# Performance work log

Measured on AMD Instinct MI355X. Metric: run time of the kernel, lower is better.

## Reference

```python
import jax, jax.numpy as jnp
import numpy as np

N_DRUG = 846
E = 64          # embedding_num
S = 1024        # neighbor_sample_size
T_LEN = 50000   # tail entity vocab
R_LEN = 100     # relation vocab
BN_EPS = 1e-5


def setup_inputs() -> dict:
    key = jax.random.key(0)
    ks = jax.random.split(key, 12)
    inp = {
        'drug_name': jnp.arange(N_DRUG, dtype=jnp.int64) if jax.config.jax_enable_x64 else jnp.arange(N_DRUG, dtype=jnp.int32),
        'adj_tail': jax.random.randint(ks[0], (N_DRUG, S), 0, T_LEN),
        'adj_relation': jax.random.randint(ks[1], (N_DRUG, S), 0, R_LEN),
        # learned parameters
        'drug_table': jax.random.normal(ks[2], (N_DRUG, E), jnp.float32),
        'rela_table': jax.random.normal(ks[3], (R_LEN, E), jnp.float32),
        'ent_table': jax.random.normal(ks[4], (T_LEN, E), jnp.float32),
        'W1': jax.random.normal(ks[5], (N_DRUG, E, E), jnp.float32),
        'b1': jax.random.normal(ks[6], (S, E), jnp.float32),
        'W2': jax.random.normal(ks[7], (N_DRUG, E, E), jnp.float32),
        'b2': jax.random.normal(ks[8], (S, E), jnp.float32),
        'lin_W': jax.random.normal(ks[9], (E, 2 * E), jnp.float32) * (6.0 / (3 * E)) ** 0.5,  # xavier-ish
        'lin_b': jnp.zeros((E,), jnp.float32),
        'bn_gamma': jnp.ones((E,), jnp.float32),
        'bn_beta': jnp.zeros((E,), jnp.float32),
    }
    return inp


def _forward(drug_table, rela_table, ent_table, W1, b1, W2, b2,
             lin_W, lin_b, bn_gamma, bn_beta,
             drug_name, adj_tail, adj_relation):
    drug_emb = drug_table[drug_name]                     # [N, E]
    rela_emb = rela_table[adj_relation]                  # [N, S, E]
    ent_emb = ent_table[adj_tail]                        # [N, S, E]

    drug_rel = drug_emb[:, None, :] * rela_emb           # [N, S, E]
    h = jax.nn.relu(jnp.einsum('nse,nef->nsf', drug_rel, W1) + b1)
    h = jnp.einsum('nse,nef->nsf', h, W2) + b2           # [N, S, E]
    score = jnp.sum(h, axis=-1)                          # [N, S]
    attn = jax.nn.softmax(score, axis=1)                 # softmax over neighbors
    weighted_ent = jnp.einsum('ns,nse->ne', attn, ent_emb)  # [N, E]

    drug_e = jnp.concatenate([weighted_ent, drug_emb], axis=1)  # [N, 2E]
    x = jax.nn.relu(drug_e @ lin_W.T + lin_b)            # [N, E]
    # BatchNorm1d in training mode: biased batch stats over the node dim
    mean = jnp.mean(x, axis=0)
    var = jnp.var(x, axis=0)
    drug_f = (x - mean) * jax.lax.rsqrt(var + BN_EPS) * bn_gamma + bn_beta
    return drug_f


def reference(drug_name, adj_tail, adj_relation, drug_table, rela_table,
              ent_table, W1, b1, W2, b2, lin_W, lin_b, bn_gamma, bn_beta):
    return _forward(drug_table, rela_table, ent_table, W1, b1, W2, b2,
                    lin_W, lin_b, bn_gamma, bn_beta,
                    drug_name, adj_tail, adj_relation)
```

## Files before the change

kernel.cpp:

```cpp
#include <hip/hip_runtime.h>

#define NDRUG 846
#define EDIM  64
#define SNB   1024
#define RLEN  100

#define XBUF_OFF  0
#define B2SUM_OFF (NDRUG*EDIM)

__global__ __launch_bounds__(256) void prep2(const float* __restrict__ b2,
                                             float* __restrict__ b2sum)
{
  int t = threadIdx.x;
  int s = blockIdx.x*64 + (t >> 2);
  int q = t & 3;
  const float4* p = reinterpret_cast<const float4*>(b2 + (size_t)s*EDIM) + q*4;
  float4 a = p[0], b = p[1], c = p[2], d = p[3];
  float v = (a.x+a.y+a.z+a.w) + (b.x+b.y+b.z+b.w)
          + (c.x+c.y+c.z+c.w) + (d.x+d.y+d.z+d.w);
  v += __shfl_xor(v, 1);
  v += __shfl_xor(v, 2);
  if (q == 0) b2sum[s] = v;
}

__global__ __launch_bounds__(256, 4) void gnn_main(
    const int*   __restrict__ adj_tail,  const int* __restrict__ adj_relation,
    const float* __restrict__ drug_table, const float* __restrict__ rela_table,
    const float* __restrict__ ent_table, const float* __restrict__ W1,
    const float* __restrict__ W2,        const float* __restrict__ b1,
    const float* __restrict__ lin_W,     const float* __restrict__ lin_b,
    const float* __restrict__ b2sum,     float* __restrict__ xbuf)
{
  __shared__ __align__(16) float lds[8080];
  float* g_s     = lds;
  float* score_s = lds + 6600;
  float* red_s   = lds + 7624;
  float* went_s  = lds + 7880;
  float* demb_s  = lds + 7944;
  float* w2sum_s = lds + 8008;
  float* mred    = lds + 8072;

  int n  = blockIdx.x;
  int t  = threadIdx.x;
  int w4 = __builtin_amdgcn_readfirstlane(t >> 6);
  int ln = t & 63;

  if (t < EDIM) demb_s[t] = drug_table[(size_t)n*EDIM + t];
  {
    int e = t >> 2, q = t & 3;
    const float4* w2p4 = reinterpret_cast<const float4*>(W2 + (size_t)n*4096);
    float4 a = w2p4[e*16 + q*4 + 0], b = w2p4[e*16 + q*4 + 1];
    float4 c = w2p4[e*16 + q*4 + 2], d = w2p4[e*16 + q*4 + 3];
    float s16 = (a.x+a.y+a.z+a.w) + (b.x+b.y+b.z+b.w)
              + (c.x+c.y+c.z+c.w) + (d.x+d.y+d.z+d.w);
    s16 += __shfl_xor(s16, 1);
    s16 += __shfl_xor(s16, 2);
    if (q == 0) w2sum_s[e] = s16;
  }
  __syncthreads();

  {
    const float* w1p   = W1 + (size_t)n*4096 + ln;
    const float* dembg = drug_table + (size_t)n*EDIM;
    int rbase = w4*25;
    float acc[25];
    {
      float w1c[32];
      #pragma unroll
      for (int e = 0; e < 32; ++e) w1c[e] = w1p[e*64] * dembg[e];
      #pragma unroll
      for (int rr = 0; rr < 25; ++rr) {
        const float* rp = rela_table + (size_t)(rbase + rr)*EDIM;
        float a = 0.f;
        #pragma unroll
        for (int e = 0; e < 32; ++e) a = fmaf(rp[e], w1c[e], a);
        acc[rr] = a;
      }
    }
    {
      float w1c[32];
      #pragma unroll
      for (int e = 0; e < 32; ++e) w1c[e] = w1p[(e+32)*64] * dembg[e+32];
      #pragma unroll
      for (int rr = 0; rr < 25; ++rr) {
        const float* rp = rela_table + (size_t)(rbase + rr)*EDIM + 32;
        float a = acc[rr];
        #pragma unroll
        for (int e = 0; e < 32; ++e) a = fmaf(rp[e], w1c[e], a);
        g_s[(rbase + rr)*66 + ln] = a;
      }
    }
  }
  __syncthreads();

  {
    int fq = ln & 3;
    int sh = t >> 2;
    float w2r[16];
    #pragma unroll
    for (int jj = 0; jj < 4; ++jj) {
      float4 v4 = *reinterpret_cast<const float4*>(w2sum_s + jj*16 + fq*4);
      w2r[jj*4+0] = v4.x; w2r[jj*4+1] = v4.y; w2r[jj*4+2] = v4.z; w2r[jj*4+3] = v4.w;
    }
    #pragma unroll
    for (int it = 0; it < 16; ++it) {
      int s   = it*64 + sh;
      int rel = adj_relation[(size_t)n*SNB + s];
      const float4* b1r = reinterpret_cast<const float4*>(b1 + (size_t)s*EDIM);
      const float2* g2  = reinterpret_cast<const float2*>(g_s + rel*66);
      float a2 = 0.f;
      #pragma unroll
      for (int jj = 0; jj < 4; ++jj) {
        float4 bv = b1r[jj*4 + fq];
        float2 ga = g2[jj*8 + fq*2];
        float2 gb = g2[jj*8 + fq*2 + 1];
        a2 = fmaf(fmaxf(ga.x + bv.x, 0.f), w2r[jj*4+0], a2);
        a2 = fmaf(fmaxf(ga.y + bv.y, 0.f), w2r[jj*4+1], a2);
        a2 = fmaf(fmaxf(gb.x + bv.z, 0.f), w2r[jj*4+2], a2);
        a2 = fmaf(fmaxf(gb.y + bv.w, 0.f), w2r[jj*4+3], a2);
      }
      a2 += __shfl_xor(a2, 1);
      a2 += __shfl_xor(a2, 2);
      if (fq == 0) score_s[s] = a2 + b2sum[s];
    }
  }
  __syncthreads();

  float av[4];
  {
    float sc[4];
    #pragma unroll
    for (int p = 0; p < 4; ++p) sc[p] = score_s[p*256 + t];
    float m = fmaxf(fmaxf(sc[0], sc[1]), fmaxf(sc[2], sc[3]));
    #pragma unroll
    for (int o = 32; o >= 1; o >>= 1) m = fmaxf(m, __shfl_xor(m, o));
    if (ln == 0) mred[w4] = m;
    __syncthreads();
    float M = fmaxf(fmaxf(mred[0], mred[1]), fmaxf(mred[2], mred[3]));
    float sum = 0.f;
    #pragma unroll
    for (int p = 0; p < 4; ++p) { av[p] = __expf(sc[p] - M); sum += av[p]; }
    #pragma unroll
    for (int o = 32; o >= 1; o >>= 1) sum += __shfl_xor(sum, o);
    if (ln == 0) mred[4 + w4] = sum;
    __syncthreads();
    float S = (mred[4] + mred[5]) + (mred[6] + mred[7]);
    float inv = 1.0f / S;
    #pragma unroll
    for (int p = 0; p < 4; ++p) av[p] *= inv;
  }

  {
    float acc4 = 0.f;
    const int* tails = adj_tail + (size_t)n*SNB;
    #pragma unroll
    for (int p = 0; p < 4; ++p) {
      unsigned long long mm = __ballot(av[p] > 2e-9f);
      int sbase = p*256 + w4*64;
      while (mm) {
        int b = __ffsll(mm) - 1; mm &= mm - 1;
        float a = __shfl(av[p], b);
        acc4 = fmaf(a, ent_table[(size_t)tails[sbase + b]*EDIM + ln], acc4);
      }
    }
    red_s[w4*64 + ln] = acc4;
  }
  __syncthreads();
  if (t < EDIM) {
    float w = ((red_s[t] + red_s[64 + t]) + (red_s[128 + t] + red_s[192 + t]));
    went_s[t] = w;
  }
  __syncthreads();

  {
    float acc = 0.f;
    const float* lw = lin_W + (size_t)ln*128 + w4*32;
    #pragma unroll
    for (int k = 0; k < 32; ++k) {
      int kk = w4*32 + k;
      float cv = (kk < 64) ? went_s[kk] : demb_s[kk - 64];
      acc = fmaf(cv, lw[k], acc);
    }
    red_s[w4*64 + ln] = acc;
  }
  __syncthreads();
  if (t < EDIM) {
    float x = lin_b[t] + (red_s[t] + red_s[64 + t]) + (red_s[128 + t] + red_s[192 + t]);
    xbuf[(size_t)n*EDIM + t] = fmaxf(x, 0.f);
  }
}

__global__ __launch_bounds__(256) void bn_kernel(
    const float* __restrict__ xbuf, const float* __restrict__ gamma,
    const float* __restrict__ beta, float* __restrict__ out)
{
  __shared__ float r1[4], r2[4];
  int e = blockIdx.x, t = threadIdx.x;
  float v[4];
  float s = 0.f, s2 = 0.f;
  #pragma unroll
  for (int k = 0; k < 4; ++k) {
    int nn = t + k*256;
    v[k] = (nn < NDRUG) ? xbuf[(size_t)nn*EDIM + e] : 0.f;
    s += v[k]; s2 += v[k]*v[k];
  }
  #pragma unroll
  for (int o = 32; o >= 1; o >>= 1) { s += __shfl_xor(s, o); s2 += __shfl_xor(s2, o); }
  if ((t & 63) == 0) { r1[t >> 6] = s; r2[t >> 6] = s2; }
  __syncthreads();
  float S  = r1[0] + r1[1] + r1[2] + r1[3];
  float S2 = r2[0] + r2[1] + r2[2] + r2[3];
  float mean = S / (float)NDRUG;
  float var  = S2 / (float)NDRUG - mean*mean;
  float sc   = gamma[e] * rsqrtf(var + 1e-5f);
  float sh   = beta[e] - mean*sc;
  #pragma unroll
  for (int k = 0; k < 4; ++k) {
    int nn = t + k*256;
    if (nn < NDRUG) out[(size_t)nn*EDIM + e] = v[k]*sc + sh;
  }
}

extern "C" void kernel_launch(void* const* d_in, const int* in_sizes, int n_in,
                              void* d_out, int out_size, void* d_ws, size_t ws_size,
                              hipStream_t stream)
{
  const int*   adj_tail   = (const int*)d_in[1];
  const int*   adj_rel    = (const int*)d_in[2];
  const float* drug_table = (const float*)d_in[3];
  const float* rela_table = (const float*)d_in[4];
  const float* ent_table  = (const float*)d_in[5];
  const float* W1         = (const float*)d_in[6];
  const float* b1         = (const float*)d_in[7];
  const float* W2         = (const float*)d_in[8];
  const float* b2         = (const float*)d_in[9];
  const float* lin_W      = (const float*)d_in[10];
  const float* lin_b      = (const float*)d_in[11];
  const float* gamma      = (const float*)d_in[12];
  const float* beta       = (const float*)d_in[13];

  float* ws    = (float*)d_ws;
  float* xbuf  = ws + XBUF_OFF;
  float* b2sum = ws + B2SUM_OFF;
  float* out   = (float*)d_out;

  hipLaunchKernelGGL(prep2, dim3(16), dim3(256), 0, stream, b2, b2sum);
  hipLaunchKernelGGL(gnn_main, dim3(NDRUG), dim3(256), 0, stream,
                     adj_tail, adj_rel, drug_table, rela_table, ent_table,
                     W1, W2, b1, lin_W, lin_b, b2sum, xbuf);
  hipLaunchKernelGGL(bn_kernel, dim3(EDIM), dim3(256), 0, stream,
                     xbuf, gamma, beta, out);
}
```

Measured before the change: 150.1 us.

## Split fused GNN kernel into prep, pairwise score, and final stages via workspace

Splits the single per-drug kernel into three. The first computes the per-relation G table using a transposed, swizzled LDS copy of the scaled relation table, and folds in the b2 reduction. The second loads G for two drugs at a time and shares each b1 row load between them while computing scores over half the neighbors per block. The third does softmax, the sparse entity gather and the linear layer. The split aims to cut redundant b1 traffic and improve the G matmul's data reuse, at the cost of writing G (about 22MB) and the scores to global memory and adding extra launches.

```diff
diff --git a/kernel.cpp b/kernel.cpp
--- a/kernel.cpp
+++ b/kernel.cpp
@@ -1,51 +1,32 @@
 #include <hip/hip_runtime.h>
 
 #define NDRUG 846
+#define NPAIR 423
 #define EDIM  64
 #define SNB   1024
 #define RLEN  100
 
-#define XBUF_OFF  0
-#define B2SUM_OFF (NDRUG*EDIM)
-
-__global__ __launch_bounds__(256) void prep2(const float* __restrict__ b2,
-                                             float* __restrict__ b2sum)
-{
-  int t = threadIdx.x;
-  int s = blockIdx.x*64 + (t >> 2);
-  int q = t & 3;
-  const float4* p = reinterpret_cast<const float4*>(b2 + (size_t)s*EDIM) + q*4;
-  float4 a = p[0], b = p[1], c = p[2], d = p[3];
-  float v = (a.x+a.y+a.z+a.w) + (b.x+b.y+b.z+b.w)
-          + (c.x+c.y+c.z+c.w) + (d.x+d.y+d.z+d.w);
-  v += __shfl_xor(v, 1);
-  v += __shfl_xor(v, 2);
-  if (q == 0) b2sum[s] = v;
-}
-
-__global__ __launch_bounds__(256, 4) void gnn_main(
-    const int*   __restrict__ adj_tail,  const int* __restrict__ adj_relation,
-    const float* __restrict__ drug_table, const float* __restrict__ rela_table,
-    const float* __restrict__ ent_table, const float* __restrict__ W1,
-    const float* __restrict__ W2,        const float* __restrict__ b1,
-    const float* __restrict__ lin_W,     const float* __restrict__ lin_b,
-    const float* __restrict__ b2sum,     float* __restrict__ xbuf)
-{
-  __shared__ __align__(16) float lds[8080];
-  float* g_s     = lds;
-  float* score_s = lds + 6600;
-  float* red_s   = lds + 7624;
-  float* went_s  = lds + 7880;
-  float* demb_s  = lds + 7944;
-  float* w2sum_s = lds + 8008;
-  float* mred    = lds + 8072;
+#define G_OFF     0
+#define SCORE_OFF (G_OFF + NDRUG*RLEN*EDIM)
+#define W2_OFF    (SCORE_OFF + NDRUG*SNB)
+#define B2_OFF    (W2_OFF + NDRUG*EDIM)
+#define XBUF_OFF  (B2_OFF + SNB)
+
+__global__ __launch_bounds__(256, 4) void k0_prep(
+    const float* __restrict__ W1, const float* __restrict__ W2,
+    const float* __restrict__ b2, const float* __restrict__ drug_table,
+    const float* __restrict__ rela_table,
+    float* __restrict__ g_ws, float* __restrict__ w2_ws,
+    float* __restrict__ b2sum_ws)
+{
+  __shared__ __align__(16) float drT[8192];
+  __shared__ float demb_s[EDIM];
 
   int n  = blockIdx.x;
   int t  = threadIdx.x;
   int w4 = __builtin_amdgcn_readfirstlane(t >> 6);
   int ln = t & 63;
 
-  if (t < EDIM) demb_s[t] = drug_table[(size_t)n*EDIM + t];
   {
     int e = t >> 2, q = t & 3;
     const float4* w2p4 = reinterpret_cast<const float4*>(W2 + (size_t)n*4096);
@@ -55,82 +36,157 @@
               + (c.x+c.y+c.z+c.w) + (d.x+d.y+d.z+d.w);
     s16 += __shfl_xor(s16, 1);
     s16 += __shfl_xor(s16, 2);
-    if (q == 0) w2sum_s[e] = s16;
-  }
-  __syncthreads();
-
-  {
-    const float* w1p   = W1 + (size_t)n*4096 + ln;
-    const float* dembg = drug_table + (size_t)n*EDIM;
-    int rbase = w4*25;
+    if (q == 0) w2_ws[n*EDIM + e] = s16;
+  }
+  if (n < 16) {
+    int sl = t >> 2, q = t & 3;
+    int s = n*64 + sl;
+    const float4* p = reinterpret_cast<const float4*>(b2 + (size_t)s*EDIM) + q*4;
+    float4 a = p[0], b = p[1], c = p[2], d = p[3];
+    float v = (a.x+a.y+a.z+a.w) + (b.x+b.y+b.z+b.w)
+            + (c.x+c.y+c.z+c.w) + (d.x+d.y+d.z+d.w);
+    v += __shfl_xor(v, 1);
+    v += __shfl_xor(v, 2);
+    if (q == 0) b2sum_ws[s] = v;
+  }
+  if (t < EDIM) demb_s[t] = drug_table[(size_t)n*EDIM + t];
+  __syncthreads();
+
+  {
+    const float4* rel4 = reinterpret_cast<const float4*>(rela_table);
+    for (int i4 = t; i4 < 1600; i4 += 256) {
+      float4 rv = rel4[i4];
+      int r  = i4 >> 4;
+      int e0 = (i4 & 15) << 2;
+      int w  = (r*41) >> 10;
+      int pos = w*32 + (r - w*25);
+      float vals[4] = {rv.x, rv.y, rv.z, rv.w};
+      #pragma unroll
+      for (int k = 0; k < 4; ++k) {
+        int e = e0 + k;
+        drT[e*128 + (pos ^ ((e & 7) << 2))] = vals[k] * demb_s[e];
+      }
+    }
+  }
+  __syncthreads();
+
+  {
     float acc[25];
-    {
-      float w1c[32];
+    #pragma unroll
+    for (int i = 0; i < 25; ++i) acc[i] = 0.f;
+    const float* w1p = W1 + (size_t)n*4096 + ln;
+    #pragma unroll 4
+    for (int e = 0; e < 64; ++e) {
+      float w1v = w1p[e*64];
+      const float* br = drT + e*128 + (w4 << 5);
+      int swz = (e & 7) << 2;
       #pragma unroll
-      for (int e = 0; e < 32; ++e) w1c[e] = w1p[e*64] * dembg[e];
-      #pragma unroll
-      for (int rr = 0; rr < 25; ++rr) {
-        const float* rp = rela_table + (size_t)(rbase + rr)*EDIM;
-        float a = 0.f;
-        #pragma unroll
-        for (int e = 0; e < 32; ++e) a = fmaf(rp[e], w1c[e], a);
-        acc[rr] = a;
+      for (int q = 0; q < 6; ++q) {
+        float4 d4 = *reinterpret_cast<const float4*>(br + ((q*4) ^ swz));
+        acc[q*4+0] = fmaf(d4.x, w1v, acc[q*4+0]);
+        acc[q*4+1] = fmaf(d4.y, w1v, acc[q*4+1]);
+        acc[q*4+2] = fmaf(d4.z, w1v, acc[q*4+2]);
+        acc[q*4+3] = fmaf(d4.w, w1v, acc[q*4+3]);
       }
-    }
-    {
-      float w1c[32];
-      #pragma unroll
-      for (int e = 0; e < 32; ++e) w1c[e] = w1p[(e+32)*64] * dembg[e+32];
-      #pragma unroll
-      for (int rr = 0; rr < 25; ++rr) {
-        const float* rp = rela_table + (size_t)(rbase + rr)*EDIM + 32;
-        float a = acc[rr];
-        #pragma unroll
-        for (int e = 0; e < 32; ++e) a = fmaf(rp[e], w1c[e], a);
-        g_s[(rbase + rr)*66 + ln] = a;
-      }
-    }
-  }
-  __syncthreads();
-
-  {
-    int fq = ln & 3;
-    int sh = t >> 2;
-    float w2r[16];
+      float4 d6 = *reinterpret_cast<const float4*>(br + (24 ^ swz));
+      acc[24] = fmaf(d6.x, w1v, acc[24]);
+    }
+    float* gp = g_ws + (size_t)n*6400 + (size_t)(w4*25)*64 + ln;
+    #pragma unroll
+    for (int rr = 0; rr < 25; ++rr) gp[rr*64] = acc[rr];
+  }
+}
+
+__global__ __launch_bounds__(256, 4) void k1_score(
+    const int*   __restrict__ adj_relation, const float* __restrict__ b1,
+    const float* __restrict__ g_ws,  const float* __restrict__ w2_ws,
+    const float* __restrict__ b2sum_ws, float* __restrict__ score_ws)
+{
+  __shared__ __align__(16) float g2[2*RLEN*65];
+  int bid = blockIdx.x;
+  int h = (bid >= 424) ? 1 : 0;
+  int p = bid - h*424;
+  if (p >= NPAIR) return;
+  int n0 = p*2;
+  int t = threadIdx.x, ln = t & 63;
+  int fq = ln & 3, sh = t >> 2;
+
+  {
+    const float4* src = reinterpret_cast<const float4*>(g_ws + (size_t)n0*6400);
+    for (int i4 = t; i4 < 3200; i4 += 256) {
+      float4 v = src[i4];
+      int row = i4 >> 4, e0 = (i4 & 15) << 2;
+      float* dst = g2 + row*65 + e0;
+      dst[0] = v.x; dst[1] = v.y; dst[2] = v.z; dst[3] = v.w;
+    }
+  }
+  float w2r[2][16];
+  #pragma unroll
+  for (int d = 0; d < 2; ++d) {
+    const float4* wp = reinterpret_cast<const float4*>(w2_ws + (size_t)(n0+d)*EDIM);
     #pragma unroll
     for (int jj = 0; jj < 4; ++jj) {
-      float4 v4 = *reinterpret_cast<const float4*>(w2sum_s + jj*16 + fq*4);
-      w2r[jj*4+0] = v4.x; w2r[jj*4+1] = v4.y; w2r[jj*4+2] = v4.z; w2r[jj*4+3] = v4.w;
-    }
-    #pragma unroll
-    for (int it = 0; it < 16; ++it) {
-      int s   = it*64 + sh;
-      int rel = adj_relation[(size_t)n*SNB + s];
-      const float4* b1r = reinterpret_cast<const float4*>(b1 + (size_t)s*EDIM);
-      const float2* g2  = reinterpret_cast<const float2*>(g_s + rel*66);
+      float4 v4 = wp[jj*4 + fq];
+      w2r[d][jj*4+0] = v4.x; w2r[d][jj*4+1] = v4.y;
+      w2r[d][jj*4+2] = v4.z; w2r[d][jj*4+3] = v4.w;
+    }
+  }
+  __syncthreads();
+
+  #pragma unroll 2
+  for (int it = 0; it < 8; ++it) {
+    int s = h*512 + it*64 + sh;
+    const float4* b1r = reinterpret_cast<const float4*>(b1 + (size_t)s*EDIM);
+    float4 bv[4];
+    #pragma unroll
+    for (int jj = 0; jj < 4; ++jj) bv[jj] = b1r[jj*4 + fq];
+    float b2v  = b2sum_ws[s];
+    int   rel0 = adj_relation[(size_t)n0*SNB + s];
+    int   rel1 = adj_relation[(size_t)(n0+1)*SNB + s];
+    #pragma unroll
+    for (int d = 0; d < 2; ++d) {
+      int rel = d ? rel1 : rel0;
+      const float* gp = g2 + (size_t)(d*RLEN + rel)*65;
       float a2 = 0.f;
       #pragma unroll
       for (int jj = 0; jj < 4; ++jj) {
-        float4 bv = b1r[jj*4 + fq];
-        float2 ga = g2[jj*8 + fq*2];
-        float2 gb = g2[jj*8 + fq*2 + 1];
-        a2 = fmaf(fmaxf(ga.x + bv.x, 0.f), w2r[jj*4+0], a2);
-        a2 = fmaf(fmaxf(ga.y + bv.y, 0.f), w2r[jj*4+1], a2);
-        a2 = fmaf(fmaxf(gb.x + bv.z, 0.f), w2r[jj*4+2], a2);
-        a2 = fmaf(fmaxf(gb.y + bv.w, 0.f), w2r[jj*4+3], a2);
+        float2 ga = *reinterpret_cast<const float2*>(gp + jj*16 + fq*4);
+        float2 gb = *reinterpret_cast<const float2*>(gp + jj*16 + fq*4 + 2);
+        a2 = fmaf(fmaxf(ga.x + bv[jj].x, 0.f), w2r[d][jj*4+0], a2);
+        a2 = fmaf(fmaxf(ga.y + bv[jj].y, 0.f), w2r[d][jj*4+1], a2);
+        a2 = fmaf(fmaxf(gb.x + bv[jj].z, 0.f), w2r[d][jj*4+2], a2);
+        a2 = fmaf(fmaxf(gb.y + bv[jj].w, 0.f), w2r[d][jj*4+3], a2);
       }
       a2 += __shfl_xor(a2, 1);
       a2 += __shfl_xor(a2, 2);
-      if (fq == 0) score_s[s] = a2 + b2sum[s];
-    }
-  }
-  __syncthreads();
+      if (fq == 0) score_ws[(size_t)(n0+d)*SNB + s] = a2 + b2v;
+    }
+  }
+}
+
+__global__ __launch_bounds__(256, 4) void k2_final(
+    const int*   __restrict__ adj_tail, const float* __restrict__ drug_table,
+    const float* __restrict__ ent_table, const float* __restrict__ lin_W,
+    const float* __restrict__ lin_b, const float* __restrict__ score_ws,
+    float* __restrict__ xbuf)
+{
+  __shared__ float red_s[256];
+  __shared__ float went_s[EDIM];
+  __shared__ float demb_s[EDIM];
+  __shared__ float mred[8];
+
+  int n  = blockIdx.x;
+  int t  = threadIdx.x;
+  int w4 = __builtin_amdgcn_readfirstlane(t >> 6);
+  int ln = t & 63;
+
+  if (t < EDIM) demb_s[t] = drug_table[(size_t)n*EDIM + t];
 
   float av[4];
   {
     float sc[4];
     #pragma unroll
-    for (int p = 0; p < 4; ++p) sc[p] = score_s[p*256 + t];
+    for (int p = 0; p < 4; ++p) sc[p] = score_ws[(size_t)n*SNB + p*256 + t];
     float m = fmaxf(fmaxf(sc[0], sc[1]), fmaxf(sc[2], sc[3]));
     #pragma unroll
     for (int o = 32; o >= 1; o >>= 1) m = fmaxf(m, __shfl_xor(m, o));
@@ -166,10 +222,8 @@
     red_s[w4*64 + ln] = acc4;
   }
   __syncthreads();
-  if (t < EDIM) {
-    float w = ((red_s[t] + red_s[64 + t]) + (red_s[128 + t] + red_s[192 + t]));
-    went_s[t] = w;
-  }
+  if (t < EDIM)
+    went_s[t] = (red_s[t] + red_s[64 + t]) + (red_s[128 + t] + red_s[192 + t]);
   __syncthreads();
 
   {
@@ -239,15 +293,20 @@
   const float* gamma      = (const float*)d_in[12];
   const float* beta       = (const float*)d_in[13];
 
-  float* ws    = (float*)d_ws;
-  float* xbuf  = ws + XBUF_OFF;
-  float* b2sum = ws + B2SUM_OFF;
-  float* out   = (float*)d_out;
-
-  hipLaunchKernelGGL(prep2, dim3(16), dim3(256), 0, stream, b2, b2sum);
-  hipLaunchKernelGGL(gnn_main, dim3(NDRUG), dim3(256), 0, stream,
-                     adj_tail, adj_rel, drug_table, rela_table, ent_table,
-                     W1, W2, b1, lin_W, lin_b, b2sum, xbuf);
+  float* ws       = (float*)d_ws;
+  float* g_ws     = ws + G_OFF;
+  float* score_ws = ws + SCORE_OFF;
+  float* w2_ws    = ws + W2_OFF;
+  float* b2sum_ws = ws + B2_OFF;
+  float* xbuf     = ws + XBUF_OFF;
+  float* out      = (float*)d_out;
+
+  hipLaunchKernelGGL(k0_prep, dim3(NDRUG), dim3(256), 0, stream,
+                     W1, W2, b2, drug_table, rela_table, g_ws, w2_ws, b2sum_ws);
+  hipLaunchKernelGGL(k1_score, dim3(848), dim3(256), 0, stream,
+                     adj_rel, b1, g_ws, w2_ws, b2sum_ws, score_ws);
+  hipLaunchKernelGGL(k2_final, dim3(NDRUG), dim3(256), 0, stream,
+                     adj_tail, drug_table, ent_table, lin_W, lin_b, score_ws, xbuf);
   hipLaunchKernelGGL(bn_kernel, dim3(EDIM), dim3(256), 0, stream,
                      xbuf, gamma, beta, out);
 }
```

Result: slower. 212.6 us (+41.6%).

## Split fused kernel into score and softmax-gather kernels with halved score blocks

Applied to the files above, without the earlier changes.

Splits the single per-drug kernel into a scoring kernel and a final kernel. The scoring kernel uses two blocks per drug, each handling half of the neighbors, and scores pass through a global workspace. W2 row sums are precomputed for all drugs in a separate prep kernel. The LDS table now uses an XOR swizzle so reads are float4 instead of padded float2. The aim is more parallelism and less per-block serial work, at the cost of redundantly computing the relation table in both halves, an extra launch, and a global round trip for scores.

```diff
diff --git a/kernel.cpp b/kernel.cpp
--- a/kernel.cpp
+++ b/kernel.cpp
@@ -5,59 +5,52 @@
 #define SNB   1024
 #define RLEN  100
 
-#define XBUF_OFF  0
-#define B2SUM_OFF (NDRUG*EDIM)
-
-__global__ __launch_bounds__(256) void prep2(const float* __restrict__ b2,
-                                             float* __restrict__ b2sum)
+#define SCORE_OFF 0
+#define W2_OFF    (SCORE_OFF + NDRUG*SNB)
+#define B2_OFF    (W2_OFF + NDRUG*EDIM)
+#define XBUF_OFF  (B2_OFF + SNB)
+
+__global__ __launch_bounds__(256) void p0_rows(
+    const float* __restrict__ W2, const float* __restrict__ b2,
+    float* __restrict__ w2_ws, float* __restrict__ b2sum_ws)
 {
   int t = threadIdx.x;
-  int s = blockIdx.x*64 + (t >> 2);
+  int row = blockIdx.x*64 + (t >> 2);
   int q = t & 3;
-  const float4* p = reinterpret_cast<const float4*>(b2 + (size_t)s*EDIM) + q*4;
+  const float* src = (row < NDRUG*EDIM)
+      ? W2 + (size_t)row*64
+      : b2 + (size_t)(row - NDRUG*EDIM)*64;
+  const float4* p = reinterpret_cast<const float4*>(src) + q*4;
   float4 a = p[0], b = p[1], c = p[2], d = p[3];
   float v = (a.x+a.y+a.z+a.w) + (b.x+b.y+b.z+b.w)
           + (c.x+c.y+c.z+c.w) + (d.x+d.y+d.z+d.w);
   v += __shfl_xor(v, 1);
   v += __shfl_xor(v, 2);
-  if (q == 0) b2sum[s] = v;
-}
-
-__global__ __launch_bounds__(256, 4) void gnn_main(
-    const int*   __restrict__ adj_tail,  const int* __restrict__ adj_relation,
+  if (q == 0) {
+    if (row < NDRUG*EDIM) w2_ws[row] = v;
+    else                  b2sum_ws[row - NDRUG*EDIM] = v;
+  }
+}
+
+__global__ __launch_bounds__(256, 4) void k1_score(
+    const int*   __restrict__ adj_relation,
     const float* __restrict__ drug_table, const float* __restrict__ rela_table,
-    const float* __restrict__ ent_table, const float* __restrict__ W1,
-    const float* __restrict__ W2,        const float* __restrict__ b1,
-    const float* __restrict__ lin_W,     const float* __restrict__ lin_b,
-    const float* __restrict__ b2sum,     float* __restrict__ xbuf)
-{
-  __shared__ __align__(16) float lds[8080];
-  float* g_s     = lds;
-  float* score_s = lds + 6600;
-  float* red_s   = lds + 7624;
-  float* went_s  = lds + 7880;
-  float* demb_s  = lds + 7944;
-  float* w2sum_s = lds + 8008;
-  float* mred    = lds + 8072;
-
-  int n  = blockIdx.x;
+    const float* __restrict__ W1, const float* __restrict__ b1,
+    const float* __restrict__ w2_ws, const float* __restrict__ b2sum_ws,
+    float* __restrict__ score_ws)
+{
+  __shared__ __align__(16) float g_s[RLEN*64];
+
+  int bid = blockIdx.x;
+  int h = (bid >= 848) ? 1 : 0;
+  int n = bid - h*848;
+  if (n >= NDRUG) return;
+
   int t  = threadIdx.x;
   int w4 = __builtin_amdgcn_readfirstlane(t >> 6);
   int ln = t & 63;
-
-  if (t < EDIM) demb_s[t] = drug_table[(size_t)n*EDIM + t];
-  {
-    int e = t >> 2, q = t & 3;
-    const float4* w2p4 = reinterpret_cast<const float4*>(W2 + (size_t)n*4096);
-    float4 a = w2p4[e*16 + q*4 + 0], b = w2p4[e*16 + q*4 + 1];
-    float4 c = w2p4[e*16 + q*4 + 2], d = w2p4[e*16 + q*4 + 3];
-    float s16 = (a.x+a.y+a.z+a.w) + (b.x+b.y+b.z+b.w)
-              + (c.x+c.y+c.z+c.w) + (d.x+d.y+d.z+d.w);
-    s16 += __shfl_xor(s16, 1);
-    s16 += __shfl_xor(s16, 2);
-    if (q == 0) w2sum_s[e] = s16;
-  }
-  __syncthreads();
+  int fq = ln & 3, sh = t >> 2;
+  int s0 = h*512;
 
   {
     const float* w1p   = W1 + (size_t)n*4096 + ln;
@@ -87,50 +80,77 @@
         float a = acc[rr];
         #pragma unroll
         for (int e = 0; e < 32; ++e) a = fmaf(rp[e], w1c[e], a);
-        g_s[(rbase + rr)*66 + ln] = a;
+        int r = rbase + rr;
+        g_s[r*64 + (((ln >> 2) ^ (r & 15)) << 2) + (ln & 3)] = a;
       }
     }
   }
-  __syncthreads();
-
-  {
-    int fq = ln & 3;
-    int sh = t >> 2;
-    float w2r[16];
+
+  float w2r[16];
+  {
+    const float4* wp = reinterpret_cast<const float4*>(w2_ws + (size_t)n*EDIM);
     #pragma unroll
     for (int jj = 0; jj < 4; ++jj) {
-      float4 v4 = *reinterpret_cast<const float4*>(w2sum_s + jj*16 + fq*4);
-      w2r[jj*4+0] = v4.x; w2r[jj*4+1] = v4.y; w2r[jj*4+2] = v4.z; w2r[jj*4+3] = v4.w;
-    }
-    #pragma unroll
-    for (int it = 0; it < 16; ++it) {
-      int s   = it*64 + sh;
-      int rel = adj_relation[(size_t)n*SNB + s];
-      const float4* b1r = reinterpret_cast<const float4*>(b1 + (size_t)s*EDIM);
-      const float2* g2  = reinterpret_cast<const float2*>(g_s + rel*66);
-      float a2 = 0.f;
-      #pragma unroll
-      for (int jj = 0; jj < 4; ++jj) {
-        float4 bv = b1r[jj*4 + fq];
-        float2 ga = g2[jj*8 + fq*2];
-        float2 gb = g2[jj*8 + fq*2 + 1];
-        a2 = fmaf(fmaxf(ga.x + bv.x, 0.f), w2r[jj*4+0], a2);
-        a2 = fmaf(fmaxf(ga.y + bv.y, 0.f), w2r[jj*4+1], a2);
-        a2 = fmaf(fmaxf(gb.x + bv.z, 0.f), w2r[jj*4+2], a2);
-        a2 = fmaf(fmaxf(gb.y + bv.w, 0.f), w2r[jj*4+3], a2);
-      }
-      a2 += __shfl_xor(a2, 1);
-      a2 += __shfl_xor(a2, 2);
-      if (fq == 0) score_s[s] = a2 + b2sum[s];
-    }
-  }
-  __syncthreads();
+      float4 v4 = wp[jj*4 + fq];
+      w2r[jj*4+0] = v4.x; w2r[jj*4+1] = v4.y;
+      w2r[jj*4+2] = v4.z; w2r[jj*4+3] = v4.w;
+    }
+  }
+  int relv[8]; float b2v[8];
+  #pragma unroll
+  for (int it = 0; it < 8; ++it) {
+    int s = s0 + it*64 + sh;
+    relv[it] = adj_relation[(size_t)n*SNB + s];
+    b2v[it]  = b2sum_ws[s];
+  }
+  __syncthreads();
+
+  #pragma unroll 2
+  for (int it = 0; it < 8; ++it) {
+    int s   = s0 + it*64 + sh;
+    int rel = relv[it];
+    int m   = rel & 15;
+    const float4* b1r   = reinterpret_cast<const float4*>(b1 + (size_t)s*EDIM);
+    const float*  gbase = g_s + rel*64;
+    float a2 = 0.f;
+    #pragma unroll
+    for (int jj = 0; jj < 4; ++jj) {
+      float4 bv = b1r[jj*4 + fq];
+      float4 gv = *reinterpret_cast<const float4*>(gbase + (((jj*4 + fq) ^ m) << 2));
+      a2 = fmaf(fmaxf(gv.x + bv.x, 0.f), w2r[jj*4+0], a2);
+      a2 = fmaf(fmaxf(gv.y + bv.y, 0.f), w2r[jj*4+1], a2);
+      a2 = fmaf(fmaxf(gv.z + bv.z, 0.f), w2r[jj*4+2], a2);
+      a2 = fmaf(fmaxf(gv.w + bv.w, 0.f), w2r[jj*4+3], a2);
+    }
+    a2 += __shfl_xor(a2, 1);
+    a2 += __shfl_xor(a2, 2);
+    if (fq == 0) score_ws[(size_t)n*SNB + s] = a2 + b2v[it];
+  }
+}
+
+__global__ __launch_bounds__(256, 4) void k2_final(
+    const int*   __restrict__ adj_tail, const float* __restrict__ drug_table,
+    const float* __restrict__ ent_table, const float* __restrict__ lin_W,
+    const float* __restrict__ lin_b, const float* __restrict__ score_ws,
+    float* __restrict__ xbuf)
+{
+  __shared__ float red_s[256];
+  __shared__ float went_s[EDIM];
+  __shared__ float demb_s[EDIM];
+  __shared__ float mred[8];
+
+  int n  = blockIdx.x;
+  int t  = threadIdx.x;
+  int w4 = __builtin_amdgcn_readfirstlane(t >> 6);
+  int ln = t & 63;
+
+  if (t < EDIM) demb_s[t] = drug_table[(size_t)n*EDIM + t];
 
   float av[4];
   {
     float sc[4];
     #pragma unroll
-    for (int p = 0; p < 4; ++p) sc[p] = score_s[p*256 + t];
+    for (int p = 0; p < 4; ++p) sc[p] = score_ws[(size_t)n*SNB + p*256 + t];
     float m = fmaxf(fmaxf(sc[0], sc[1]), fmaxf(sc[2], sc[3]));
     #pragma unroll
     for (int o = 32; o >= 1; o >>= 1) m = fmaxf(m, __shfl_xor(m, o));
@@ -166,10 +186,8 @@
     red_s[w4*64 + ln] = acc4;
   }
   __syncthreads();
-  if (t < EDIM) {
-    float w = ((red_s[t] + red_s[64 + t]) + (red_s[128 + t] + red_s[192 + t]));
-    went_s[t] = w;
-  }
+  if (t < EDIM)
+    went_s[t] = (red_s[t] + red_s[64 + t]) + (red_s[128 + t] + red_s[192 + t]);
   __syncthreads();
 
   {
@@ -239,15 +257,21 @@
   const float* gamma      = (const float*)d_in[12];
   const float* beta       = (const float*)d_in[13];
 
-  float* ws    = (float*)d_ws;
-  float* xbuf  = ws + XBUF_OFF;
-  float* b2sum = ws + B2SUM_OFF;
-  float* out   = (float*)d_out;
-
-  hipLaunchKernelGGL(prep2, dim3(16), dim3(256), 0, stream, b2, b2sum);
-  hipLaunchKernelGGL(gnn_main, dim3(NDRUG), dim3(256), 0, stream,
-                     adj_tail, adj_rel, drug_table, rela_table, ent_table,
-                     W1, W2, b1, lin_W, lin_b, b2sum, xbuf);
+  float* ws       = (float*)d_ws;
+  float* score_ws = ws + SCORE_OFF;
+  float* w2_ws    = ws + W2_OFF;
+  float* b2sum_ws = ws + B2_OFF;
+  float* xbuf     = ws + XBUF_OFF;
+  float* out      = (float*)d_out;
+
+  hipLaunchKernelGGL(p0_rows, dim3(862), dim3(256), 0, stream,
+                     W2, b2, w2_ws, b2sum_ws);
+  hipLaunchKernelGGL(k1_score, dim3(1696), dim3(256), 0, stream,
+                     adj_rel, drug_table, rela_table, W1, b1,
+                     w2_ws, b2sum_ws, score_ws);
+  hipLaunchKernelGGL(k2_final, dim3(NDRUG), dim3(256), 0, stream,
+                     adj_tail, drug_table, ent_table, lin_W, lin_b,
+                     score_ws, xbuf);
   hipLaunchKernelGGL(bn_kernel, dim3(EDIM), dim3(256), 0, stream,
                      xbuf, gamma, beta, out);
 }
```

New measurement: 171.6 us. 1.14x slower.
